# Optimization experiments

Measured on AMD Instinct MI355X. Metric: run time of the kernel, lower is better.

## Reference

```python
import jax, jax.numpy as jnp
import numpy as np

B, T_H, T_W, S_H, S_W = 64, 8, 8, 20, 20
DIM, HEADS = 768, 12
L = 2 * T_H * T_W + S_H * S_W  # 528


def setup_inputs() -> dict:
    key = jax.random.key(0)
    ks = jax.random.split(key, 6)
    sd = 0.02
    return {
        "x": jax.random.normal(ks[0], (B, L, DIM), jnp.float32),
        "Wq": jax.random.normal(ks[1], (DIM, DIM), jnp.float32) * sd,
        "Wk": jax.random.normal(ks[2], (DIM, DIM), jnp.float32) * sd,
        "Wv": jax.random.normal(ks[3], (DIM, DIM), jnp.float32) * sd,
        "Wp": jax.random.normal(ks[4], (DIM, DIM), jnp.float32) * sd,
        "bp": jnp.zeros((DIM,), jnp.float32),
        "t_h": T_H, "t_w": T_W, "s_h": S_H, "s_w": S_W,
    }


def _heads(y, h):
    b, t, d = y.shape
    return y.reshape(b, t, h, d // h).transpose(0, 2, 1, 3)  # b h t d


def _merge(y):
    b, h, t, d = y.shape
    return y.transpose(0, 2, 1, 3).reshape(b, t, h * d)


def _attn(q, k, v, scale):
    s = jnp.einsum("bhld,bhtd->bhlt", q, k) * scale
    p = jax.nn.softmax(s, axis=-1)
    return jnp.einsum("bhlt,bhtd->bhld", p, v)


def reference(x, Wq, Wk, Wv, Wp, bp, t_h, t_w, s_h, s_w):
    # forward_conv with default path is identity: q = k = v = x
    dim = Wq.shape[1]
    scale = dim ** (-0.5)  # NOTE: full dim_out, faithful to original
    q = _heads(x @ Wq, HEADS)
    k = _heads(x @ Wk, HEADS)
    v = _heads(x @ Wv, HEADS)
    Lt = t_h * t_w
    q_t, q_ot, q_s = q[:, :, :Lt], q[:, :, Lt:2 * Lt], q[:, :, 2 * Lt:]
    k12 = k[:, :, :2 * Lt]  # template+online keys
    v12 = v[:, :, :2 * Lt]
    x_t = _attn(q_t, k12, v12, scale)
    x_ot = _attn(q_ot, k12, v12, scale)
    x_s = _attn(q_s, k, v, scale)  # search attends to everything
    out = jnp.concatenate([_merge(x_t), _merge(x_ot), _merge(x_s)], axis=1)
    return out @ Wp + bp
```

## Files before the change

kernel.cpp:

```cpp
#include <hip/hip_runtime.h>
#include <stdint.h>

typedef __attribute__((ext_vector_type(8))) short bf16x8;
typedef __attribute__((ext_vector_type(4))) float f32x4;
typedef unsigned short ushort_t;
typedef unsigned int u32;
typedef const __attribute__((address_space(1))) u32* gp1_t;
typedef __attribute__((address_space(3))) u32* lp3_t;

#define MFMA(a,b,c) __builtin_amdgcn_mfma_f32_16x16x32_bf16((a),(b),(c),0,0,0)

static constexpr int BATCH = 64, LQ = 528, DIM = 768, NH = 12, DH = 64;
static constexpr int MTOK = BATCH * LQ;
static constexpr int VTP  = 544;
static constexpr float QSCALE = (float)(0.03608439182435161 * 1.4426950408889634);

__device__ __forceinline__ ushort_t f2bf(float f) {
  u32 u = __float_as_uint(f);
  u = (u + 0x7fffu + ((u >> 16) & 1u)) >> 16;
  return (ushort_t)u;
}
__device__ __forceinline__ u32 cvtpk(float a, float b) {
  u32 r;
  asm("v_cvt_pk_bf16_f32 %0, %1, %2" : "=v"(r) : "v"(a), "v"(b));
  return r;
}

__global__ __launch_bounds__(256) void k_convert(
    const float* __restrict__ x, ushort_t* __restrict__ xb,
    const float* __restrict__ w0, const float* __restrict__ w1,
    const float* __restrict__ w2, const float* __restrict__ w3,
    ushort_t* __restrict__ o0, ushort_t* __restrict__ o1,
    ushort_t* __restrict__ o2, ushort_t* __restrict__ o3) {
  __shared__ ushort_t t[64][65];
  if (blockIdx.x < 25344) {
    int i = blockIdx.x * 256 + threadIdx.x;
    float4 v = ((const float4*)x)[i];
    ushort4 o;
    o.x = f2bf(v.x); o.y = f2bf(v.y); o.z = f2bf(v.z); o.w = f2bf(v.w);
    ((ushort4*)xb)[i] = o;
    return;
  }
  int bid = blockIdx.x - 25344;
  int kx = bid % 12, ny = (bid / 12) % 12, mid = bid / 144;
  const float* src = (mid == 0) ? w0 : (mid == 1) ? w1 : (mid == 2) ? w2 : w3;
  ushort_t* dst = (mid == 0) ? o0 : (mid == 1) ? o1 : (mid == 2) ? o2 : o3;
  int k0 = kx * 64, n0 = ny * 64;
  int c = threadIdx.x & 63, rr = threadIdx.x >> 6;
#pragma unroll
  for (int p = 0; p < 16; p++) {
    int r = p * 4 + rr;
    t[c][r] = f2bf(src[(size_t)(k0 + r) * DIM + n0 + c]);
  }
  __syncthreads();
#pragma unroll
  for (int p = 0; p < 16; p++) {
    int r = p * 4 + rr;
    dst[(size_t)(n0 + r) * DIM + k0 + c] = t[r][c];
  }
}

__global__ __launch_bounds__(256, 2) void k_gemm_qkv(
    const ushort_t* __restrict__ A, const ushort_t* __restrict__ wq,
    const ushort_t* __restrict__ wk, const ushort_t* __restrict__ wv,
    ushort_t* __restrict__ Qb, ushort_t* __restrict__ Kb, ushort_t* __restrict__ Vtb) {
  const int id = blockIdx.x, xcd = id & 7, s = id >> 3;
  const int mT = xcd * 33 + s / 18, t = s % 18, w = t / 6, nT = t % 6;
  const ushort_t* Bt = (w == 0) ? wq : (w == 1) ? wk : wv;

  __shared__ ushort_t at[128 * 64];
  __shared__ ushort_t bt[128 * 64];
  const int tid = threadIdx.x;
  const int wv_ = tid >> 6, lane = tid & 63;
  const int lane15 = lane & 15, quad = lane >> 4;
  const int mw = (wv_ & 1) * 64, nw = (wv_ >> 1) * 64;

  f32x4 acc[4][4];
#pragma unroll
  for (int i = 0; i < 4; i++)
#pragma unroll
    for (int j = 0; j < 4; j++) acc[i][j] = (f32x4)0.0f;

  const int lrow = lane >> 3;
  const int lchunk = lane & 7;

  for (int kb = 0; kb < 768; kb += 64) {
#pragma unroll
    for (int i = 0; i < 4; i++) {
      int r0 = wv_ * 32 + i * 8;
      int lr = r0 + lrow;
      size_t off = (size_t)(mT * 128 + lr) * 768 + kb + ((lchunk ^ (lr & 7)) << 3);
      __builtin_amdgcn_global_load_lds((gp1_t)(A + off), (lp3_t)(&at[r0 * 64]), 16, 0, 0);
    }
#pragma unroll
    for (int i = 0; i < 4; i++) {
      int r0 = wv_ * 32 + i * 8;
      int lr = r0 + lrow;
      size_t off = (size_t)(nT * 128 + lr) * 768 + kb + ((lchunk ^ (lr & 7)) << 3);
      __builtin_amdgcn_global_load_lds((gp1_t)(Bt + off), (lp3_t)(&bt[r0 * 64]), 16, 0, 0);
    }
    __syncthreads();
#pragma unroll
    for (int h = 0; h < 2; h++) {
      bf16x8 af[4], bf[4];
#pragma unroll
      for (int mi = 0; mi < 4; mi++) {
        int row = mw + mi * 16 + lane15;
        af[mi] = *(const bf16x8*)&at[row * 64 + (((h * 4 + quad) ^ (row & 7)) << 3)];
      }
#pragma unroll
      for (int ni = 0; ni < 4; ni++) {
        int row = nw + ni * 16 + lane15;
        bf[ni] = *(const bf16x8*)&bt[row * 64 + (((h * 4 + quad) ^ (row & 7)) << 3)];
      }
#pragma unroll
      for (int mi = 0; mi < 4; mi++)
#pragma unroll
        for (int ni = 0; ni < 4; ni++)
          acc[mi][ni] = MFMA(af[mi], bf[ni], acc[mi][ni]);
    }
    __syncthreads();
  }

  const float scale = (w == 0) ? QSCALE : 1.0f;
  ushort_t* Cqk = (w == 0) ? Qb : Kb;
#pragma unroll
  for (int mi = 0; mi < 4; mi++) {
#pragma unroll
    for (int r = 0; r < 4; r++) {
      int m = mT * 128 + mw + mi * 16 + quad * 4 + r;
      int b = m / 528, lt = m - b * 528;
#pragma unroll
      for (int ni = 0; ni < 4; ni++) {
        int n = nT * 128 + nw + ni * 16 + lane15;
        float v = acc[mi][ni][r];
        if (w < 2) {
          Cqk[(((size_t)(b * 12 + (n >> 6)) * 528 + lt) << 6) + (n & 63)] = f2bf(v * scale);
        } else {
          Vtb[((size_t)(b * 12 + (n >> 6)) * 64 + (n & 63)) * VTP + lt] = f2bf(v);
        }
      }
    }
  }
}

__global__ __launch_bounds__(256, 2) void k_gemm_out(const ushort_t* __restrict__ A,
                                                     const ushort_t* __restrict__ Bt,
                                                     float* __restrict__ C,
                                                     const float* __restrict__ bias) {
  const int id = blockIdx.x, xcd = id & 7, s = id >> 3;
  const int mT = xcd * 33 + s / 6, nT = s % 6;

  __shared__ ushort_t at[128 * 64];
  __shared__ ushort_t bt[128 * 64];
  const int tid = threadIdx.x;
  const int wv_ = tid >> 6, lane = tid & 63;
  const int lane15 = lane & 15, quad = lane >> 4;
  const int mw = (wv_ & 1) * 64, nw = (wv_ >> 1) * 64;

  f32x4 acc[4][4];
#pragma unroll
  for (int i = 0; i < 4; i++)
#pragma unroll
    for (int j = 0; j < 4; j++) acc[i][j] = (f32x4)0.0f;

  const int lrow = lane >> 3;
  const int lchunk = lane & 7;

  for (int kb = 0; kb < 768; kb += 64) {
#pragma unroll
    for (int i = 0; i < 4; i++) {
      int r0 = wv_ * 32 + i * 8;
      int lr = r0 + lrow;
      int grow = mT * 128 + lr;
      int gk = kb + ((lchunk ^ (lr & 7)) << 3);
      int b = grow / 528, ltk = grow - b * 528;
      size_t off = (((size_t)(b * 12 + (gk >> 6)) * 528 + ltk) << 6) + (gk & 63);
      __builtin_amdgcn_global_load_lds((gp1_t)(A + off), (lp3_t)(&at[r0 * 64]), 16, 0, 0);
    }
#pragma unroll
    for (int i = 0; i < 4; i++) {
      int r0 = wv_ * 32 + i * 8;
      int lr = r0 + lrow;
      size_t off = (size_t)(nT * 128 + lr) * 768 + kb + ((lchunk ^ (lr & 7)) << 3);
      __builtin_amdgcn_global_load_lds((gp1_t)(Bt + off), (lp3_t)(&bt[r0 * 64]), 16, 0, 0);
    }
    __syncthreads();
#pragma unroll
    for (int h = 0; h < 2; h++) {
      bf16x8 af[4], bf[4];
#pragma unroll
      for (int mi = 0; mi < 4; mi++) {
        int row = mw + mi * 16 + lane15;
        af[mi] = *(const bf16x8*)&at[row * 64 + (((h * 4 + quad) ^ (row & 7)) << 3)];
      }
#pragma unroll
      for (int ni = 0; ni < 4; ni++) {
        int row = nw + ni * 16 + lane15;
        bf[ni] = *(const bf16x8*)&bt[row * 64 + (((h * 4 + quad) ^ (row & 7)) << 3)];
      }
#pragma unroll
      for (int mi = 0; mi < 4; mi++)
#pragma unroll
        for (int ni = 0; ni < 4; ni++)
          acc[mi][ni] = MFMA(af[mi], bf[ni], acc[mi][ni]);
    }
    __syncthreads();
  }

#pragma unroll
  for (int mi = 0; mi < 4; mi++) {
#pragma unroll
    for (int r = 0; r < 4; r++) {
      int m = mT * 128 + mw + mi * 16 + quad * 4 + r;
#pragma unroll
      for (int ni = 0; ni < 4; ni++) {
        int n = nT * 128 + nw + ni * 16 + lane15;
        C[(size_t)m * 768 + n] = acc[mi][ni][r] + bias[n];
      }
    }
  }
}

__global__ __launch_bounds__(256, 3) void k_attn(ushort_t* __restrict__ Q,
                                                 const ushort_t* __restrict__ K,
                                                 const ushort_t* __restrict__ Vt) {
  const int tid = threadIdx.x;
  const int wv = tid >> 6, lane = tid & 63;
  const int lane15 = lane & 15, quad = lane >> 4;
  const int b = blockIdx.x, xcd = b & 7, slot = b >> 3;
  const int g = slot / 17, r = slot - g * 17;
  const int bh0 = (xcd * 24 + g) * 4;

  bf16x8 ones;
#pragma unroll
  for (int i = 0; i < 8; i++) ones[i] = (short)0x3F80;

  const int krp = ((lane15 >> 2) << 3) + (lane15 & 3);

  if (r < 16) {
    const int sub = r & 3;
    const int bh = bh0 + (r >> 2);
    const bool light = (sub == 3);
    const int rows0 = light ? (wv * 32) : (128 + sub * 128 + wv * 32);
    const int kend = light ? 128 : 544;

    ushort_t* Qb = Q + (size_t)bh * LQ * DH;
    const ushort_t* Kbh = K + (size_t)bh * LQ * DH;
    const ushort_t* Vbh = Vt + (size_t)bh * DH * VTP;

    bf16x8 aq[2][2];
#pragma unroll
    for (int mt = 0; mt < 2; mt++)
#pragma unroll
      for (int h = 0; h < 2; h++)
        aq[mt][h] = *(const bf16x8*)&Qb[(size_t)(rows0 + mt * 16 + lane15) * DH + h * 32 + quad * 8];

    f32x4 o[2][4], sm[2];
#pragma unroll
    for (int mt = 0; mt < 2; mt++) {
      sm[mt] = (f32x4)0.0f;
#pragma unroll
      for (int dt = 0; dt < 4; dt++) o[mt][dt] = (f32x4)0.0f;
    }

    const ushort_t* kbase = Kbh + (size_t)krp * DH + quad * 8;
    const ushort_t* vbase = Vbh + (size_t)lane15 * VTP + quad * 8;

    for (int kc = 0; kc < kend; kc += 32) {
      bf16x8 kf[2][2], vf[4];
#pragma unroll
      for (int ss = 0; ss < 2; ss++) {
        const ushort_t* p = kbase + (size_t)(kc + ss * 4) * DH;
        kf[ss][0] = *(const bf16x8*)&p[0];
        kf[ss][1] = *(const bf16x8*)&p[32];
      }
#pragma unroll
      for (int dt = 0; dt < 4; dt++)
        vf[dt] = *(const bf16x8*)&vbase[(size_t)dt * 16 * VTP + kc];

      const bool maskl = (kc == 512) && (quad >= 2);
#pragma unroll
      for (int mt = 0; mt < 2; mt++) {
        f32x4 c0 = (f32x4)0.0f, c1 = (f32x4)0.0f;
        c0 = MFMA(kf[0][0], aq[mt][0], c0);
        c0 = MFMA(kf[0][1], aq[mt][1], c0);
        c1 = MFMA(kf[1][0], aq[mt][0], c1);
        c1 = MFMA(kf[1][1], aq[mt][1], c1);
        float e[8];
#pragma unroll
        for (int rr = 0; rr < 4; rr++) {
          e[rr]     = exp2f(maskl ? -30.0f : c0[rr]);
          e[4 + rr] = exp2f(maskl ? -30.0f : c1[rr]);
        }
        union { bf16x8 v; u32 w[4]; } pb;
        pb.w[0] = cvtpk(e[0], e[1]);
        pb.w[1] = cvtpk(e[2], e[3]);
        pb.w[2] = cvtpk(e[4], e[5]);
        pb.w[3] = cvtpk(e[6], e[7]);
        sm[mt] = MFMA(ones, pb.v, sm[mt]);
#pragma unroll
        for (int dt = 0; dt < 4; dt++)
          o[mt][dt] = MFMA(vf[dt], pb.v, o[mt][dt]);
      }
    }

#pragma unroll
    for (int mt = 0; mt < 2; mt++) {
      float inv = 1.0f / sm[mt][0];
      ushort_t* orow = &Qb[(size_t)(rows0 + mt * 16 + lane15) * DH];
#pragma unroll
      for (int dt = 0; dt < 4; dt++) {
        uint2 st;
        st.x = cvtpk(o[mt][dt][0] * inv, o[mt][dt][1] * inv);
        st.y = cvtpk(o[mt][dt][2] * inv, o[mt][dt][3] * inv);
        *(uint2*)&orow[dt * 16 + quad * 4] = st;
      }
    }
  } else {
    const int bh = bh0 + wv;
    ushort_t* Qb = Q + (size_t)bh * LQ * DH;
    const ushort_t* Kbh = K + (size_t)bh * LQ * DH;
    const ushort_t* Vbh = Vt + (size_t)bh * DH * VTP;

    bf16x8 aq[2];
#pragma unroll
    for (int h = 0; h < 2; h++)
      aq[h] = *(const bf16x8*)&Qb[(size_t)(512 + lane15) * DH + h * 32 + quad * 8];

    f32x4 o[4], sm = (f32x4)0.0f;
#pragma unroll
    for (int dt = 0; dt < 4; dt++) o[dt] = (f32x4)0.0f;

    const ushort_t* kbase = Kbh + (size_t)krp * DH + quad * 8;
    const ushort_t* vbase = Vbh + (size_t)lane15 * VTP + quad * 8;

    for (int kc = 0; kc < 528; kc += 32) {
      bf16x8 kf[2][2], vf[4];
#pragma unroll
      for (int ss = 0; ss < 2; ss++) {
        const ushort_t* p = kbase + (size_t)(kc + ss * 4) * DH;
        kf[ss][0] = *(const bf16x8*)&p[0];
        kf[ss][1] = *(const bf16x8*)&p[32];
      }
#pragma unroll
      for (int dt = 0; dt < 4; dt++)
        vf[dt] = *(const bf16x8*)&vbase[(size_t)dt * 16 * VTP + kc];

      f32x4 c0 = (f32x4)0.0f, c1 = (f32x4)0.0f;
      c0 = MFMA(kf[0][0], aq[0], c0);
      c0 = MFMA(kf[0][1], aq[1], c0);
      c1 = MFMA(kf[1][0], aq[0], c1);
      c1 = MFMA(kf[1][1], aq[1], c1);
      const bool maskl = (kc == 512) && (quad >= 2);
      float e[8];
#pragma unroll
      for (int rr = 0; rr < 4; rr++) {
        e[rr]     = exp2f(maskl ? -30.0f : c0[rr]);
        e[4 + rr] = exp2f(maskl ? -30.0f : c1[rr]);
      }
      union { bf16x8 v; u32 w[4]; } pb;
      pb.w[0] = cvtpk(e[0], e[1]);
      pb.w[1] = cvtpk(e[2], e[3]);
      pb.w[2] = cvtpk(e[4], e[5]);
      pb.w[3] = cvtpk(e[6], e[7]);
      sm = MFMA(ones, pb.v, sm);
#pragma unroll
      for (int dt = 0; dt < 4; dt++)
        o[dt] = MFMA(vf[dt], pb.v, o[dt]);
    }

    float inv = 1.0f / sm[0];
    ushort_t* orow = &Qb[(size_t)(512 + lane15) * DH];
#pragma unroll
    for (int dt = 0; dt < 4; dt++) {
      uint2 st;
      st.x = cvtpk(o[dt][0] * inv, o[dt][1] * inv);
      st.y = cvtpk(o[dt][2] * inv, o[dt][3] * inv);
      *(uint2*)&orow[dt * 16 + quad * 4] = st;
    }
  }
}

extern "C" void kernel_launch(void* const* d_in, const int* in_sizes, int n_in,
                              void* d_out, int out_size, void* d_ws, size_t ws_size,
                              hipStream_t stream) {
  const float* x = (const float*)d_in[0];
  const float* Wq = (const float*)d_in[1];
  const float* Wk = (const float*)d_in[2];
  const float* Wv = (const float*)d_in[3];
  const float* Wp = (const float*)d_in[4];
  const float* bp = (const float*)d_in[5];
  float* out = (float*)d_out;

  char* ws = (char*)d_ws;
  size_t off = 0;
  auto alloc = [&](size_t bytes) {
    void* p = ws + off;
    off += (bytes + 255) & ~(size_t)255;
    return p;
  };
  ushort_t* xb = (ushort_t*)alloc((size_t)MTOK * DIM * 2);
  ushort_t* wtq = (ushort_t*)alloc((size_t)DIM * DIM * 2);
  ushort_t* wtk = (ushort_t*)alloc((size_t)DIM * DIM * 2);
  ushort_t* wtv = (ushort_t*)alloc((size_t)DIM * DIM * 2);
  ushort_t* wtp = (ushort_t*)alloc((size_t)DIM * DIM * 2);
  ushort_t* Qb = (ushort_t*)alloc((size_t)MTOK * DIM * 2);
  ushort_t* Kb = (ushort_t*)alloc((size_t)MTOK * DIM * 2);
  ushort_t* Vtb = (ushort_t*)alloc((size_t)BATCH * NH * DH * VTP * 2);
  (void)ws_size; (void)in_sizes; (void)n_in; (void)out_size;

  k_convert<<<25920, 256, 0, stream>>>(x, xb, Wq, Wk, Wv, Wp, wtq, wtk, wtv, wtp);
  k_gemm_qkv<<<4752, 256, 0, stream>>>(xb, wtq, wtk, wtv, Qb, Kb, Vtb);
  k_attn<<<3264, 256, 0, stream>>>(Qb, Kb, Vtb);
  k_gemm_out<<<1584, 256, 0, stream>>>(Qb, wtp, out, bp);
}
```

Baseline: 578.1 us.

## Stage K/V tiles through swizzled LDS with double-buffered async loads

In the attention kernel, the K and V tiles are now loaded cooperatively by the whole block into shared memory with global_load_lds. The four waves previously each fetched the same K/V from global memory; now they share one copy. Loads go into a two-deep buffer so the next 64-key block is fetched while the current one is computed, and XOR swizzles avoid LDS bank conflicts on the fragment reads. The cost is 32KB of LDS per block plus a barrier per key block, and correctness depends on the barriers waiting for the async LDS loads to finish.

Result: faster. 479.2 us (-17.1%).

```diff
diff --git a/kernel.cpp b/kernel.cpp
--- a/kernel.cpp
+++ b/kernel.cpp
@@ -25,6 +25,8 @@
   asm("v_cvt_pk_bf16_f32 %0, %1, %2" : "=v"(r) : "v"(a), "v"(b));
   return r;
 }
+__device__ __forceinline__ int swzK(int r) { return (r & 3) | (((r >> 3) & 1) << 2); }
+__device__ __forceinline__ int swzV(int d) { return (d >> 2) & 3; }
 
 __global__ __launch_bounds__(256) void k_convert(
     const float* __restrict__ x, ushort_t* __restrict__ xb,
@@ -225,6 +227,8 @@
 __global__ __launch_bounds__(256, 3) void k_attn(ushort_t* __restrict__ Q,
                                                  const ushort_t* __restrict__ K,
                                                  const ushort_t* __restrict__ Vt) {
+  __shared__ ushort_t Ksh[2][2][32 * 64];
+  __shared__ ushort_t Vsh[2][2][64 * 32];
   const int tid = threadIdx.x;
   const int wv = tid >> 6, lane = tid & 63;
   const int lane15 = lane & 15, quad = lane >> 4;
@@ -243,7 +247,7 @@
     const int bh = bh0 + (r >> 2);
     const bool light = (sub == 3);
     const int rows0 = light ? (wv * 32) : (128 + sub * 128 + wv * 32);
-    const int kend = light ? 128 : 544;
+    const int nbig = light ? 2 : 8;
 
     ushort_t* Qb = Q + (size_t)bh * LQ * DH;
     const ushort_t* Kbh = K + (size_t)bh * LQ * DH;
@@ -264,22 +268,34 @@
       for (int dt = 0; dt < 4; dt++) o[mt][dt] = (f32x4)0.0f;
     }
 
-    const ushort_t* kbase = Kbh + (size_t)krp * DH + quad * 8;
-    const ushort_t* vbase = Vbh + (size_t)lane15 * VTP + quad * 8;
-
-    for (int kc = 0; kc < kend; kc += 32) {
+    auto stageKV = [&](int buf, int sc, int kc) {
+      {
+        int rr = tid >> 3, u = tid & 7;
+        const ushort_t* src = Kbh + (size_t)(kc + rr) * DH + ((u ^ swzK(rr)) << 3);
+        __builtin_amdgcn_global_load_lds((gp1_t)src, (lp3_t)&Ksh[buf][sc][(wv * 8) * 64], 16, 0, 0);
+      }
+      {
+        int d = tid >> 2, cc = tid & 3;
+        const ushort_t* src = Vbh + (size_t)d * VTP + kc + ((cc ^ swzV(d)) << 3);
+        __builtin_amdgcn_global_load_lds((gp1_t)src, (lp3_t)&Vsh[buf][sc][(wv * 16) * 32], 16, 0, 0);
+      }
+    };
+
+    auto do_chunk = [&](int buf, int sc, bool domask) {
       bf16x8 kf[2][2], vf[4];
 #pragma unroll
       for (int ss = 0; ss < 2; ss++) {
-        const ushort_t* p = kbase + (size_t)(kc + ss * 4) * DH;
-        kf[ss][0] = *(const bf16x8*)&p[0];
-        kf[ss][1] = *(const bf16x8*)&p[32];
-      }
-#pragma unroll
-      for (int dt = 0; dt < 4; dt++)
-        vf[dt] = *(const bf16x8*)&vbase[(size_t)dt * 16 * VTP + kc];
-
-      const bool maskl = (kc == 512) && (quad >= 2);
+        int kr = krp + ss * 4;
+#pragma unroll
+        for (int h = 0; h < 2; h++)
+          kf[ss][h] = *(const bf16x8*)&Ksh[buf][sc][kr * 64 + (((h * 4 + quad) ^ swzK(kr)) << 3)];
+      }
+#pragma unroll
+      for (int dt = 0; dt < 4; dt++) {
+        int d = dt * 16 + lane15;
+        vf[dt] = *(const bf16x8*)&Vsh[buf][sc][d * 32 + ((quad ^ swzV(d)) << 3)];
+      }
+      const bool maskl = domask && (quad >= 2);
 #pragma unroll
       for (int mt = 0; mt < 2; mt++) {
         f32x4 c0 = (f32x4)0.0f, c1 = (f32x4)0.0f;
@@ -303,6 +319,25 @@
         for (int dt = 0; dt < 4; dt++)
           o[mt][dt] = MFMA(vf[dt], pb.v, o[mt][dt]);
       }
+    };
+
+    stageKV(0, 0, 0);
+    stageKV(0, 1, 32);
+    for (int bc = 0; bc < nbig; bc++) {
+      __syncthreads();
+      const int nb = bc + 1;
+      if (nb < nbig) {
+        stageKV(nb & 1, 0, nb * 64);
+        stageKV(nb & 1, 1, nb * 64 + 32);
+      } else if (!light) {
+        stageKV(nb & 1, 0, 512);
+      }
+      do_chunk(bc & 1, 0, false);
+      do_chunk(bc & 1, 1, false);
+    }
+    if (!light) {
+      __syncthreads();
+      do_chunk(0, 0, true);
     }
 
 #pragma unroll
```
